# Kernel tuning notes

Measured on AMD Instinct MI355X. Metric: run time of the kernel, lower is better.

Reference implementation:

```python
import jax, jax.numpy as jnp
import numpy as np

B, N, D, H, L = 64, 512, 10, 256, 128  # batch, max_size(nodes), node_dim, hidden, latent
AA, SS, ATOM = 20, 7, 5
K = 2  # conv kernel size
L_KLD = 1e-3


def _lin(k, i, o, s=0.02):
    k1, k2 = jax.random.split(k)
    return jax.random.normal(k1, (i, o), jnp.float32) * s, jax.random.normal(k2, (o,), jnp.float32) * s


def setup_inputs() -> dict:
    key = jax.random.key(0)
    ks = iter(jax.random.split(key, 40))
    nk = lambda: next(ks)
    x = jax.random.normal(nk(), (B, N, D), jnp.float32)
    aa = jax.random.randint(nk(), (B, N), 0, AA + 1).astype(jnp.float32)  # 0 = pad -> ignore_idx
    ss = jax.random.randint(nk(), (B, N), 0, SS + 1).astype(jnp.float32)
    x = x.at[:, :, 0].set(aa).at[:, :, 1].set(ss)
    adj = (jax.random.uniform(nk(), (B, N, N)) < 0.1).astype(jnp.float32)  # sparse binary adjacency
    node_mask = jax.random.randint(nk(), (B, N), 0, 2).astype(bool)
    eps = jax.random.uniform(nk(), (B, N, L), jnp.float32)  # torch.rand_like -> uniform
    W_rel, b_rel = _lin(nk(), D, H)
    W_root, _ = _lin(nk(), D, H)  # lin_root has no bias in DenseSAGEConv
    W_mu, b_mu = _lin(nk(), H, L)
    W_lv, b_lv = _lin(nk(), H, L)
    Wx1, bx1 = _lin(nk(), L, 512); Wx2, bx2 = _lin(nk(), 512, 512); Wx3, bx3 = _lin(nk(), 512, H)
    Wa1, ba1 = _lin(nk(), L, 512); Wa2, ba2 = _lin(nk(), 512, 512); Wa3, ba3 = _lin(nk(), 512, H)
    Wc1 = jax.random.normal(nk(), (256, N, K), jnp.float32) * 0.02; bc1 = jnp.zeros((256,), jnp.float32)
    Wc2 = jax.random.normal(nk(), (N, 256, K), jnp.float32) * 0.02; bc2 = jnp.zeros((N,), jnp.float32)
    W_fcx, b_fcx = _lin(nk(), H, AA * SS)
    W_fca, b_fca = _lin(nk(), H, ATOM)
    W_fcj, b_fcj = _lin(nk(), L - 2 * (K - 1), N)  # cnn out len: 128->127->126
    return dict(x=x, adj=adj, node_mask=node_mask, eps=eps, W_rel=W_rel, b_rel=b_rel, W_root=W_root,
                W_mu=W_mu, b_mu=b_mu, W_lv=W_lv, b_lv=b_lv,
                Wx1=Wx1, bx1=bx1, Wx2=Wx2, bx2=bx2, Wx3=Wx3, bx3=bx3,
                Wa1=Wa1, ba1=ba1, Wa2=Wa2, ba2=ba2, Wa3=Wa3, ba3=ba3,
                Wc1=Wc1, bc1=bc1, Wc2=Wc2, bc2=bc2,
                W_fcx=W_fcx, b_fcx=b_fcx, W_fca=W_fca, b_fca=b_fca, W_fcj=W_fcj, b_fcj=b_fcj)


def reference(x, adj, node_mask, eps, W_rel, b_rel, W_root, W_mu, b_mu, W_lv, b_lv,
              Wx1, bx1, Wx2, bx2, Wx3, bx3, Wa1, ba1, Wa2, ba2, Wa3, ba3,
              Wc1, bc1, Wc2, bc2, W_fcx, b_fcx, W_fca, b_fca, W_fcj, b_fcj):
    relu = jax.nn.relu
    # --- encode: DenseSAGEConv(x, adj, mask) ---
    deg = jnp.clip(jnp.sum(adj, axis=-1, keepdims=True), 1.0, None)
    agg = jnp.einsum('bij,bjd->bid', adj, x) / deg           # [B,N,D]
    h = agg @ W_rel + b_rel + x @ W_root                      # [B,N,H]
    h = h * node_mask[..., None].astype(h.dtype)
    h = relu(h)
    mu = h @ W_mu + b_mu
    lv = h @ W_lv + b_lv
    z = mu + eps * jnp.exp(0.5 * lv)                          # [B,N,L]
    # --- decode ---
    hx = relu(relu(z @ Wx1 + bx1) @ Wx2 + bx2) @ Wx3 + bx3    # gen_x MLP
    ha = relu(relu(z @ Wa1 + ba1) @ Wa2 + ba2) @ Wa3 + ba3    # gen_x_atomic MLP
    dn = ('NCH', 'OIH', 'NCH')
    c = relu(jax.lax.conv_general_dilated(z, Wc1, (1,), 'VALID', dimension_numbers=dn) + bc1[None, :, None])
    c = relu(jax.lax.conv_general_dilated(c, Wc2, (1,), 'VALID', dimension_numbers=dn) + bc2[None, :, None])
    out_x_class = hx @ W_fcx + b_fcx                          # [B,N,AA*SS]
    out_x_atom = ha @ W_fca + b_fca                           # [B,N,ATOM]
    out_adj = c @ W_fcj + b_fcj                               # [B,N,126]@[126,N] -> [B,N,N]
    # --- VAE loss (vectorized _input_classes / _binary_adjacency) ---
    mapping = ((x[..., 1] - 1.0) * AA + (x[..., 0] - 1.0)).astype(jnp.int32)  # [B,N]
    valid = mapping >= 0
    logp = jax.nn.log_softmax(out_x_class, axis=-1)
    ce = -jnp.take_along_axis(logp, jnp.clip(mapping, 0)[..., None], axis=-1)[..., 0]
    ce = jnp.mean(jnp.where(valid, ce, 0.0))
    pair = node_mask[:, :, None] & node_mask[:, None, :]
    eye = jnp.eye(adj.shape[1], dtype=bool)[None]
    adj_bin = (pair & (eye | (adj > 0))).astype(out_adj.dtype)
    l = out_adj
    bce = jnp.mean(jnp.maximum(l, 0.0) - l * adj_bin + jnp.log1p(jnp.exp(-jnp.abs(l))))
    mse = jnp.mean((out_x_atom - x[:, :, ATOM:]) ** 2)
    kl = -0.5 * jnp.sum(1.0 + lv - mu ** 2 - jnp.exp(lv))
    sg = jax.lax.stop_gradient
    beta = jnp.abs((sg(ce) + sg(bce)) / sg(mse))
    loss = ce + beta * mse + bce + L_KLD * kl
    return (loss, out_x_class, out_x_atom, out_adj)
```

## Files before the change

### kernel.cpp

```cpp
#include <hip/hip_runtime.h>
#include <hip/hip_bf16.h>
#include <cstdint>

using bf16x8 = __attribute__((ext_vector_type(8))) __bf16;
using floatx4 = __attribute__((ext_vector_type(4))) float;
typedef unsigned short ushort;

#define Nn  512
#define Dd  10
#define Hh  256
#define Ll  128
#define CLS 140
#define ROWS 32768
#define CH  16384

#define OUT_CLASS 1ull
#define OUT_ATOM  4587521ull
#define OUT_ADJ   4751361ull

#define T1_OFF 12ull
#define T2_OFF (12ull + 16777216ull)
#define HX_OFF (12ull + 33554432ull)
#define WT_OFF 41943068ull
#define AXS_OFF 45088780ull
#define Z_OFF  50331644ull

static __device__ __forceinline__ ushort bfb(float v) {
    __hip_bfloat16 h = __float2bfloat16(v);
    return *reinterpret_cast<ushort*>(&h);
}
static __device__ __forceinline__ float fbf(ushort u) {
    __hip_bfloat16 h = *reinterpret_cast<__hip_bfloat16*>(&u);
    return __bfloat162float(h);
}
static __device__ __forceinline__ unsigned pk2(float a, float b) {
    return (unsigned)bfb(a) | ((unsigned)bfb(b) << 16);
}

struct PDesc { const float* src; ushort* dst; int srcR, srcC, Cp, Kp, tile0, mode; };
struct PTable { PDesc d[12]; };

__global__ __launch_bounds__(256) void prep_kernel(PTable tab) {
    __shared__ float tile[32][33];
    int bt = blockIdx.x, tid = threadIdx.x;
    int di = 0;
    #pragma unroll
    for (int i = 1; i < 12; ++i) if (bt >= tab.d[i].tile0) di = i;
    PDesc d = tab.d[di];
    int lt = bt - d.tile0;
    if (d.mode == 1) {
        long base = (long)lt * 8192;
        const float* s = d.src;
        ushort* o = d.dst;
        for (int i = tid; i < 2048; i += 256) {
            long idx = base + (long)i * 4;
            float4 v = *(const float4*)&s[idx];
            unsigned u0 = pk2(v.x, v.y), u1 = pk2(v.z, v.w);
            *(uint2*)&o[idx] = (uint2){u0, u1};
        }
        return;
    }
    int tilesK = (d.Kp + 31) >> 5;
    int k0 = (lt % tilesK) << 5, n0 = (lt / tilesK) << 5;
    int tx = tid & 31, ty = tid >> 5;
    for (int ky = ty; ky < 32; ky += 8) {
        int k = k0 + ky, n = n0 + tx;
        float v = (k < d.srcR && n < d.srcC) ? d.src[(size_t)k * d.srcC + n] : 0.f;
        tile[ky][tx] = v;
    }
    __syncthreads();
    for (int ny = ty; ny < 32; ny += 8) {
        int n = n0 + ny, k = k0 + tx;
        if (n < d.Cp && k < d.Kp) d.dst[(size_t)n * d.Kp + k] = bfb(tile[tx][ny]);
    }
}

__global__ __launch_bounds__(256, 8) void agg_kernel(
    const float* __restrict__ adj, const float* __restrict__ x,
    float* __restrict__ axs_g)
{
    __shared__ float4 xs4[1536];
    float* xs = (float*)xs4;
    int tid = threadIdx.x;
    int rowbase = blockIdx.x * 16;
    int b = rowbase >> 9, rowloc = rowbase & 511;
    const float* xb = x + (size_t)b * 5120;
    for (int e = tid; e < 6144; e += 256) {
        int j = e / 12, d = e - j * 12;
        xs[e] = (d < 10) ? xb[j * 10 + d] : 0.f;
    }
    __syncthreads();
    int g = tid >> 4, l16 = tid & 15;
    int row = rowbase + g;
    size_t arow = (size_t)row * Nn;
    float accv[10] = {};
    float deg = 0.f;
    for (int it = 0; it < 32; ++it) {
        int j = l16 + (it << 4);
        float a = adj[arow + j];
        if (a != 0.f) {
            deg += a;
            float4 v0 = xs4[j * 3 + 0];
            float4 v1 = xs4[j * 3 + 1];
            float4 v2 = xs4[j * 3 + 2];
            accv[0] += a * v0.x; accv[1] += a * v0.y;
            accv[2] += a * v0.z; accv[3] += a * v0.w;
            accv[4] += a * v1.x; accv[5] += a * v1.y;
            accv[6] += a * v1.z; accv[7] += a * v1.w;
            accv[8] += a * v2.x; accv[9] += a * v2.y;
        }
    }
    #pragma unroll
    for (int o = 8; o > 0; o >>= 1) {
        deg += __shfl_xor(deg, o);
        #pragma unroll
        for (int d = 0; d < 10; ++d) accv[d] += __shfl_xor(accv[d], o);
    }
    float* orow = axs_g + (size_t)row * 20;
    if (l16 == 0) {
        float dg = fmaxf(deg, 1.f);
        #pragma unroll
        for (int d = 0; d < 10; ++d) orow[d] = accv[d] / dg;
    }
    if (l16 < 10) orow[10 + l16] = xs[(rowloc + g) * 12 + l16];
}

__global__ __launch_bounds__(256) void enc2_kernel(
    const float* __restrict__ axs_g,
    const float* __restrict__ Wrel, const float* __restrict__ brel,
    const float* __restrict__ Wroot, const int* __restrict__ nmask,
    const ushort* __restrict__ Wtmu, const float* __restrict__ bmu,
    const ushort* __restrict__ Wtlv, const float* __restrict__ blv,
    const float* __restrict__ eps, float* __restrict__ Z,
    double* __restrict__ acc_kl)
{
    __shared__ float sml[4096];
    __shared__ ushort hsb[16 * 264];
    __shared__ float axs[16][20];
    __shared__ float skred[4];
    int tid = threadIdx.x;
    int rowbase = blockIdx.x * 16;

    for (int e = tid; e < 320; e += 256) ((float*)axs)[e] = axs_g[(size_t)rowbase * 20 + e];
    __syncthreads();

    {
        int c = tid;
        float hacc[16];
        float bb = brel[c];
        #pragma unroll
        for (int r = 0; r < 16; ++r) hacc[r] = bb;
        #pragma unroll
        for (int d = 0; d < 10; ++d) {
            float wr = Wrel[d * Hh + c], wo = Wroot[d * Hh + c];
            #pragma unroll
            for (int r = 0; r < 16; ++r)
                hacc[r] += axs[r][d] * wr + axs[r][10 + d] * wo;
        }
        #pragma unroll
        for (int r = 0; r < 16; ++r) {
            float v = (nmask[rowbase + r] != 0) ? hacc[r] : 0.f;
            hsb[r * 264 + c] = bfb(fmaxf(v, 0.f));
        }
    }
    __syncthreads();

    {
        int lane = tid & 63, wid = tid >> 6;
        int l15 = lane & 15, quad = lane >> 4;
        int half = wid >> 1;
        const ushort* Wt = half ? Wtlv : Wtmu;
        const float* bv = half ? blv : bmu;
        #pragma unroll
        for (int i = 0; i < 4; ++i) {
            int ct = (wid & 1) * 4 + i;
            floatx4 a = (floatx4){0.f, 0.f, 0.f, 0.f};
            #pragma unroll
            for (int k0 = 0; k0 < 8; ++k0) {
                bf16x8 af = __builtin_bit_cast(bf16x8,
                    *(const uint4*)(hsb + l15 * 264 + k0 * 32 + quad * 8));
                bf16x8 bfr = __builtin_bit_cast(bf16x8,
                    *(const uint4*)(Wt + (size_t)(ct * 16 + l15) * 256 + k0 * 32 + quad * 8));
                a = __builtin_amdgcn_mfma_f32_16x16x32_bf16(af, bfr, a, 0, 0, 0);
            }
            int col = ct * 16 + l15;
            float bvv = bv[col];
            #pragma unroll
            for (int r4 = 0; r4 < 4; ++r4) {
                int r = quad * 4 + r4;
                sml[half * 2048 + r * 128 + col] = a[r4] + bvv;
            }
        }
    }
    __syncthreads();

    {
        float kt = 0.f;
        #pragma unroll
        for (int i = 0; i < 8; ++i) {
            int e = tid + i * 256;
            float mu = sml[e], lv = sml[2048 + e];
            float ee = eps[(size_t)rowbase * Ll + e];
            Z[(size_t)rowbase * Ll + e] = mu + ee * expf(0.5f * lv);
            kt += 1.f + lv - mu * mu - expf(lv);
        }
        #pragma unroll
        for (int o = 32; o > 0; o >>= 1) kt += __shfl_xor(kt, o);
        if ((tid & 63) == 0) skred[tid >> 6] = kt;
    }
    __syncthreads();
    if (tid == 0) atomicAdd(acc_kl, (double)(skred[0] + skred[1] + skred[2] + skred[3]));
}

__global__ __launch_bounds__(256) void mgemm_kernel(const void* __restrict__ A, int a_bf16,
                                                    const ushort* __restrict__ Bt,
                                                    const float* __restrict__ bias,
                                                    void* __restrict__ Cp, int c_fp32,
                                                    int N, int K, int ldc, int relu) {
    __shared__ uint4 AsRaw[640];
    __shared__ uint4 BsRaw[640];
    ushort* As = (ushort*)AsRaw;
    ushort* Bs = (ushort*)BsRaw;
    int tid = threadIdx.x;
    int row0 = blockIdx.y << 7, col0 = blockIdx.x << 7;
    int lane = tid & 63, wid = tid >> 6;
    int wm = (wid >> 1) * 64, wn = (wid & 1) * 64;
    int l15 = lane & 15, quad = lane >> 4;
    floatx4 acc[4][4];
    #pragma unroll
    for (int i = 0; i < 4; ++i)
        #pragma unroll
        for (int j = 0; j < 4; ++j) acc[i][j] = (floatx4){0.f, 0.f, 0.f, 0.f};
    int am = tid & 127, aseg = tid >> 7;
    for (int k0 = 0; k0 < K; k0 += 32) {
        {
            uint4* dst = (uint4*)(As + am * 40 + aseg * 16);
            if (a_bf16) {
                const uint4* ap = (const uint4*)((const ushort*)A + (size_t)(row0 + am) * K + k0 + aseg * 16);
                dst[0] = ap[0]; dst[1] = ap[1];
            } else {
                const float4* ap = (const float4*)((const float*)A + (size_t)(row0 + am) * K + k0 + aseg * 16);
                float4 f0 = ap[0], f1 = ap[1], f2 = ap[2], f3 = ap[3];
                dst[0] = (uint4){pk2(f0.x, f0.y), pk2(f0.z, f0.w), pk2(f1.x, f1.y), pk2(f1.z, f1.w)};
                dst[1] = (uint4){pk2(f2.x, f2.y), pk2(f2.z, f2.w), pk2(f3.x, f3.y), pk2(f3.z, f3.w)};
            }
        }
        {
            const uint4* bp = (const uint4*)(Bt + (size_t)(col0 + am) * K + k0 + aseg * 16);
            uint4* dst = (uint4*)(Bs + am * 40 + aseg * 16);
            dst[0] = bp[0]; dst[1] = bp[1];
        }
        __syncthreads();
        bf16x8 af[4], bfv[4];
        #pragma unroll
        for (int mt = 0; mt < 4; ++mt)
            af[mt] = __builtin_bit_cast(bf16x8, *(const uint4*)(As + (wm + mt * 16 + l15) * 40 + quad * 8));
        #pragma unroll
        for (int nt = 0; nt < 4; ++nt)
            bfv[nt] = __builtin_bit_cast(bf16x8, *(const uint4*)(Bs + (wn + nt * 16 + l15) * 40 + quad * 8));
        #pragma unroll
        for (int mt = 0; mt < 4; ++mt)
            #pragma unroll
            for (int nt = 0; nt < 4; ++nt)
                acc[mt][nt] = __builtin_amdgcn_mfma_f32_16x16x32_bf16(af[mt], bfv[nt], acc[mt][nt], 0, 0, 0);
        __syncthreads();
    }
    #pragma unroll
    for (int nt = 0; nt < 4; ++nt) {
        int n = col0 + wn + nt * 16 + l15;
        float bv = bias[n];
        #pragma unroll
        for (int mt = 0; mt < 4; ++mt)
            #pragma unroll
            for (int r = 0; r < 4; ++r) {
                size_t m = row0 + wm + mt * 16 + quad * 4 + r;
                float v = acc[mt][nt][r] + bv;
                if (relu) v = fmaxf(v, 0.f);
                if (c_fp32) ((float*)Cp)[m * ldc + n] = v;
                else ((ushort*)Cp)[m * ldc + n] = bfb(v);
            }
    }
}

__global__ __launch_bounds__(256) void convmfma_kernel(const void* __restrict__ X, int x_bf16,
                                                       long xBS,
                                                       const ushort* __restrict__ Ab,
                                                       const float* __restrict__ bias,
                                                       ushort* __restrict__ Y,
                                                       int Cout, int K, int Tout) {
    __shared__ uint4 AsRaw[640];
    __shared__ uint4 BsRaw[640];
    ushort* As = (ushort*)AsRaw;
    ushort* Bs = (ushort*)BsRaw;
    int tid = threadIdx.x, bz = blockIdx.z;
    int row0 = blockIdx.y << 7;
    int lane = tid & 63, wid = tid >> 6;
    int wm = (wid >> 1) * 64, wn = (wid & 1) * 64;
    int l15 = lane & 15, quad = lane >> 4;
    floatx4 acc[4][4];
    #pragma unroll
    for (int i = 0; i < 4; ++i)
        #pragma unroll
        for (int j = 0; j < 4; ++j) acc[i][j] = (floatx4){0.f, 0.f, 0.f, 0.f};
    int am = tid & 127, aseg = tid >> 7;
    int tnext = (am + 1 > 127) ? 127 : am + 1;
    for (int k0 = 0; k0 < K; k0 += 32) {
        {
            const uint4* ap = (const uint4*)(Ab + (size_t)(row0 + am) * K + k0 + aseg * 16);
            uint4* dst = (uint4*)(As + am * 40 + aseg * 16);
            dst[0] = ap[0]; dst[1] = ap[1];
        }
        {
            unsigned r[8];
            if (x_bf16) {
                const ushort* Xb = (const ushort*)X + (size_t)bz * xBS;
                #pragma unroll
                for (int q = 0; q < 8; ++q) {
                    int kk = k0 + aseg * 16 + 2 * q, i = kk >> 1;
                    r[q] = (unsigned)Xb[i * 128 + am] | ((unsigned)Xb[i * 128 + tnext] << 16);
                }
            } else {
                const float* Xf = (const float*)X + (size_t)bz * xBS;
                #pragma unroll
                for (int q = 0; q < 8; ++q) {
                    int kk = k0 + aseg * 16 + 2 * q, i = kk >> 1;
                    r[q] = pk2(Xf[i * 128 + am], Xf[i * 128 + tnext]);
                }
            }
            uint4* dst = (uint4*)(Bs + am * 40 + aseg * 16);
            dst[0] = (uint4){r[0], r[1], r[2], r[3]};
            dst[1] = (uint4){r[4], r[5], r[6], r[7]};
        }
        __syncthreads();
        bf16x8 af[4], bfv[4];
        #pragma unroll
        for (int mt = 0; mt < 4; ++mt)
            af[mt] = __builtin_bit_cast(bf16x8, *(const uint4*)(As + (wm + mt * 16 + l15) * 40 + quad * 8));
        #pragma unroll
        for (int nt = 0; nt < 4; ++nt)
            bfv[nt] = __builtin_bit_cast(bf16x8, *(const uint4*)(Bs + (wn + nt * 16 + l15) * 40 + quad * 8));
        #pragma unroll
        for (int mt = 0; mt < 4; ++mt)
            #pragma unroll
            for (int nt = 0; nt < 4; ++nt)
                acc[mt][nt] = __builtin_amdgcn_mfma_f32_16x16x32_bf16(af[mt], bfv[nt], acc[mt][nt], 0, 0, 0);
        __syncthreads();
    }
    #pragma unroll
    for (int mt = 0; mt < 4; ++mt)
        #pragma unroll
        for (int r = 0; r < 4; ++r) {
            int m = row0 + wm + mt * 16 + quad * 4 + r;
            float bv = bias[m];
            #pragma unroll
            for (int nt = 0; nt < 4; ++nt) {
                int col = wn + nt * 16 + l15;
                float v = fmaxf(acc[mt][nt][r] + bv, 0.f);
                if (col >= Tout) v = 0.f;
                Y[((size_t)bz * Cout + m) * 128 + col] = bfb(v);
            }
        }
}

__global__ __launch_bounds__(256) void ce_kernel(const ushort* __restrict__ hx,
                                                 const ushort* __restrict__ Wt,
                                                 const float* __restrict__ bfcx,
                                                 const float* __restrict__ x,
                                                 float* __restrict__ out_class,
                                                 double* __restrict__ acc_ce,
                                                 int row0) {
    __shared__ ushort hxb[16 * 264];
    __shared__ float slog[16][144];
    __shared__ float sce[16];
    int tid = threadIdx.x;
    int lbase = blockIdx.x * 16;
    for (int e = tid; e < 512; e += 256) {
        int r = e >> 5, seg = e & 31;
        *(uint4*)(hxb + r * 264 + seg * 8) = *(const uint4*)(hx + (size_t)(lbase + r) * 256 + seg * 8);
    }
    __syncthreads();
    int lane = tid & 63, wid = tid >> 6, l15 = lane & 15, quad = lane >> 4;
    for (int ct = wid; ct < 9; ct += 4) {
        floatx4 a = (floatx4){0.f, 0.f, 0.f, 0.f};
        #pragma unroll
        for (int k0 = 0; k0 < 8; ++k0) {
            bf16x8 af = __builtin_bit_cast(bf16x8, *(const uint4*)(hxb + l15 * 264 + k0 * 32 + quad * 8));
            bf16x8 bfr = __builtin_bit_cast(bf16x8, *(const uint4*)(Wt + (size_t)(ct * 16 + l15) * 256 + k0 * 32 + quad * 8));
            a = __builtin_amdgcn_mfma_f32_16x16x32_bf16(af, bfr, a, 0, 0, 0);
        }
        int col = ct * 16 + l15;
        float bv = (col < CLS) ? bfcx[col] : 0.f;
        #pragma unroll
        for (int r4 = 0; r4 < 4; ++r4) {
            int r = quad * 4 + r4;
            float v = a[r4] + bv;
            slog[r][col] = v;
            if (col < CLS) out_class[(size_t)(row0 + lbase + r) * CLS + col] = v;
        }
    }
    __syncthreads();
    #pragma unroll
    for (int rr = 0; rr < 4; ++rr) {
        int r = wid * 4 + rr;
        float m = -1e30f;
        for (int j = lane; j < CLS; j += 64) m = fmaxf(m, slog[r][j]);
        #pragma unroll
        for (int o = 32; o > 0; o >>= 1) m = fmaxf(m, __shfl_xor(m, o));
        float s = 0.f;
        for (int j = lane; j < CLS; j += 64) s += expf(slog[r][j] - m);
        #pragma unroll
        for (int o = 32; o > 0; o >>= 1) s += __shfl_xor(s, o);
        if (lane == 0) {
            size_t grow = (size_t)row0 + lbase + r;
            float aa = x[grow * Dd + 0];
            float ss = x[grow * Dd + 1];
            int mapping = (int)((ss - 1.f) * 20.f + (aa - 1.f));
            int idx = mapping > 0 ? mapping : 0;
            float ce = -(slog[r][idx] - m - logf(s));
            sce[r] = (mapping < 0) ? 0.f : ce;
        }
    }
    __syncthreads();
    if (tid == 0) {
        float t = 0.f;
        #pragma unroll
        for (int r = 0; r < 16; ++r) t += sce[r];
        atomicAdd(acc_ce, (double)t);
    }
}

__global__ __launch_bounds__(256) void atom_kernel(const ushort* __restrict__ ha,
                                                   const float* __restrict__ Wfca,
                                                   const float* __restrict__ bfca,
                                                   const float* __restrict__ x,
                                                   float* __restrict__ out_atom,
                                                   double* __restrict__ acc_mse,
                                                   int row0) {
    __shared__ double sred[4];
    int tid = threadIdx.x;
    int wid = tid >> 6, lane = tid & 63;
    int rowblk = blockIdx.x * 64;
    double msum = 0.0;
    for (int rr = 0; rr < 16; ++rr) {
        int lrow = rowblk + wid * 16 + rr;
        size_t grow = (size_t)row0 + lrow;
        float acc[5] = {};
        for (int k = lane; k < 256; k += 64) {
            float hv = fbf(ha[(size_t)lrow * Hh + k]);
            #pragma unroll
            for (int o = 0; o < 5; ++o) acc[o] = fmaf(hv, Wfca[k * 5 + o], acc[o]);
        }
        #pragma unroll
        for (int o = 0; o < 5; ++o)
            #pragma unroll
            for (int s = 32; s > 0; s >>= 1) acc[o] += __shfl_xor(acc[o], s);
        if (lane == 0) {
            float ms = 0.f;
            #pragma unroll
            for (int o = 0; o < 5; ++o) {
                float v = acc[o] + bfca[o];
                out_atom[grow * 5 + o] = v;
                float d = v - x[grow * Dd + 5 + o];
                ms += d * d;
            }
            msum += (double)ms;
        }
    }
    if (lane == 0) sred[wid] = msum;
    __syncthreads();
    if (tid == 0) atomicAdd(acc_mse, sred[0] + sred[1] + sred[2] + sred[3]);
}

__global__ __launch_bounds__(256) void bce_kernel(const float* __restrict__ out_adj,
                                                  const float* __restrict__ adj,
                                                  const int* __restrict__ nmask,
                                                  double* __restrict__ acc_bce) {
    __shared__ float sred[4];
    int tid = threadIdx.x;
    float bsum = 0.f;
    for (size_t e = (size_t)blockIdx.x * 256 + tid; e < 16777216ull; e += (size_t)gridDim.x * 256) {
        float l = out_adj[e];
        size_t grow = e >> 9;
        int col = (int)(e & 511);
        int gb = (int)(grow >> 9), n = (int)(grow & 511);
        int mn = nmask[grow];
        int cm = nmask[(size_t)gb * 512 + col];
        float a = adj[e];
        bool abin = (mn != 0) && (cm != 0) && ((col == n) || (a > 0.f));
        bsum += fmaxf(l, 0.f) - (abin ? l : 0.f) + log1pf(expf(-fabsf(l)));
    }
    #pragma unroll
    for (int o = 32; o > 0; o >>= 1) bsum += __shfl_xor(bsum, o);
    if ((tid & 63) == 0) sred[tid >> 6] = bsum;
    __syncthreads();
    if (tid == 0) atomicAdd(acc_bce, (double)(sred[0] + sred[1] + sred[2] + sred[3]));
}

__global__ __launch_bounds__(256) void convgemm_kernel(const float* __restrict__ X,
                                                       const float* __restrict__ Wc,
                                                       const float* __restrict__ bias,
                                                       float* __restrict__ Y,
                                                       int Cin, int Tin, int Cout) {
    __shared__ float As[16][68];
    __shared__ float Bs[16][68];
    int K = Cin * 2, Tout = Tin - 1;
    int tid = threadIdx.x, bz = blockIdx.z;
    const float* Xb = X + (size_t)bz * Cin * Tin;
    int m0 = blockIdx.y << 6, col0 = blockIdx.x << 6;
    int tx = tid & 15, ty = tid >> 4;
    float acc[4][4] = {};
    int sm = tid & 63, sks = (tid >> 6) << 2;
    int bkk = tid >> 4, btof = (tid & 15) << 2;
    for (int k0 = 0; k0 < K; k0 += 16) {
        float4 av = *(const float4*)&Wc[(size_t)(m0 + sm) * K + k0 + sks];
        As[sks + 0][sm] = av.x; As[sks + 1][sm] = av.y;
        As[sks + 2][sm] = av.z; As[sks + 3][sm] = av.w;
        {
            int kg = k0 + bkk, i = kg >> 1, par = kg & 1;
            const float* xr = Xb + (size_t)i * Tin;
            #pragma unroll
            for (int j = 0; j < 4; ++j) {
                int t = col0 + btof + j + par;
                if (t > Tin - 1) t = Tin - 1;
                Bs[bkk][btof + j] = xr[t];
            }
        }
        __syncthreads();
        #pragma unroll
        for (int kk = 0; kk < 16; ++kk) {
            float4 a4 = *(const float4*)&As[kk][ty << 2];
            float4 b4 = *(const float4*)&Bs[kk][tx << 2];
            float a[4] = {a4.x, a4.y, a4.z, a4.w};
            float bb[4] = {b4.x, b4.y, b4.z, b4.w};
            #pragma unroll
            for (int i = 0; i < 4; ++i)
                #pragma unroll
                for (int j = 0; j < 4; ++j)
                    acc[i][j] = fmaf(a[i], bb[j], acc[i][j]);
        }
        __syncthreads();
    }
    #pragma unroll
    for (int i = 0; i < 4; ++i) {
        int m = m0 + (ty << 2) + i;
        float bv = bias[m];
        #pragma unroll
        for (int j = 0; j < 4; ++j) {
            int col = col0 + (tx << 2) + j;
            if (col < Tout)
                Y[((size_t)bz * Cout + m) * Tout + col] = fmaxf(acc[i][j] + bv, 0.f);
        }
    }
}

__global__ __launch_bounds__(256) void adjbce_kernel(const float* __restrict__ c2,
                                                     const float* __restrict__ Wfcj,
                                                     const float* __restrict__ bfcj,
                                                     const float* __restrict__ adj,
                                                     const int* __restrict__ nmask,
                                                     float* __restrict__ out_adj,
                                                     double* __restrict__ acc_bce,
                                                     int b0) {
    __shared__ float cs[8][126];
    __shared__ int smn[8];
    __shared__ float sred[4];
    int tid = threadIdx.x;
    int lbase = blockIdx.x * 8;
    size_t growbase = (size_t)b0 * Nn + lbase;
    int gb = (int)(growbase >> 9);
    for (int e = tid; e < 8 * 126; e += 256) {
        int r = e / 126, k = e - r * 126;
        cs[r][k] = c2[(size_t)(lbase + r) * 126 + k];
    }
    if (tid < 8) smn[tid] = nmask[growbase + tid];
    __syncthreads();
    int j0 = tid, j1 = tid + 256;
    float l0[8], l1[8];
    float bj0 = bfcj[j0], bj1 = bfcj[j1];
    #pragma unroll
    for (int r = 0; r < 8; ++r) { l0[r] = bj0; l1[r] = bj1; }
    for (int k = 0; k < 126; ++k) {
        float w0 = Wfcj[k * Nn + j0];
        float w1 = Wfcj[k * Nn + j1];
        #pragma unroll
        for (int r = 0; r < 8; ++r) {
            float cv = cs[r][k];
            l0[r] = fmaf(cv, w0, l0[r]);
            l1[r] = fmaf(cv, w1, l1[r]);
        }
    }
    int cm0 = nmask[(size_t)(gb << 9) + j0];
    int cm1 = nmask[(size_t)(gb << 9) + j1];
    float bsum = 0.f;
    #pragma unroll
    for (int r = 0; r < 8; ++r) {
        size_t grow = growbase + r;
        int n = (int)(grow & 511);
        int mn = smn[r];
        float a0 = adj[grow * Nn + j0];
        float a1 = adj[grow * Nn + j1];
        out_adj[grow * Nn + j0] = l0[r];
        out_adj[grow * Nn + j1] = l1[r];
        bool ab0 = (mn != 0) && (cm0 != 0) && ((j0 == n) || (a0 > 0.f));
        bool ab1 = (mn != 0) && (cm1 != 0) && ((j1 == n) || (a1 > 0.f));
        bsum += fmaxf(l0[r], 0.f) - (ab0 ? l0[r] : 0.f) + log1pf(expf(-fabsf(l0[r])));
        bsum += fmaxf(l1[r], 0.f) - (ab1 ? l1[r] : 0.f) + log1pf(expf(-fabsf(l1[r])));
    }
    #pragma unroll
    for (int o = 32; o > 0; o >>= 1) bsum += __shfl_xor(bsum, o);
    if ((tid & 63) == 0) sred[tid >> 6] = bsum;
    __syncthreads();
    if (tid == 0) atomicAdd(acc_bce, (double)(sred[0] + sred[1] + sred[2] + sred[3]));
}

__global__ void loss_kernel(const double* __restrict__ acc, float* __restrict__ out) {
    double ce  = acc[0] / 32768.0;
    double bce = acc[1] / 16777216.0;
    double mse = acc[2] / 163840.0;
    double kl  = -0.5 * acc[3];
    double bm = (mse != 0.0) ? fabs(ce + bce) : 0.0;
    out[0] = (float)(ce + bm + bce + 1e-3 * kl);
}

extern "C" void kernel_launch(void* const* d_in, const int* in_sizes, int n_in,
                              void* d_out, int out_size, void* d_ws, size_t ws_size,
                              hipStream_t stream) {
    const float* x      = (const float*)d_in[0];
    const float* adj    = (const float*)d_in[1];
    const int*   nmask  = (const int*)d_in[2];
    const float* eps    = (const float*)d_in[3];
    const float* W_rel  = (const float*)d_in[4];
    const float* b_rel  = (const float*)d_in[5];
    const float* W_root = (const float*)d_in[6];
    const float* W_mu   = (const float*)d_in[7];
    const float* b_mu   = (const float*)d_in[8];
    const float* W_lv   = (const float*)d_in[9];
    const float* b_lv   = (const float*)d_in[10];
    const float* Wx1    = (const float*)d_in[11];
    const float* bx1    = (const float*)d_in[12];
    const float* Wx2    = (const float*)d_in[13];
    const float* bx2    = (const float*)d_in[14];
    const float* Wx3    = (const float*)d_in[15];
    const float* bx3    = (const float*)d_in[16];
    const float* Wa1    = (const float*)d_in[17];
    const float* ba1    = (const float*)d_in[18];
    const float* Wa2    = (const float*)d_in[19];
    const float* ba2    = (const float*)d_in[20];
    const float* Wa3    = (const float*)d_in[21];
    const float* ba3    = (const float*)d_in[22];
    const float* Wc1    = (const float*)d_in[23];
    const float* bc1    = (const float*)d_in[24];
    const float* Wc2    = (const float*)d_in[25];
    const float* bc2    = (const float*)d_in[26];
    const float* W_fcx  = (const float*)d_in[27];
    const float* b_fcx  = (const float*)d_in[28];
    const float* W_fca  = (const float*)d_in[29];
    const float* b_fca  = (const float*)d_in[30];
    const float* W_fcj  = (const float*)d_in[31];
    const float* b_fcj  = (const float*)d_in[32];

    float* out = (float*)d_out;
    char* region = (char*)(out + OUT_ADJ);
    ushort* t1 = (ushort*)(region + T1_OFF);
    ushort* t2 = (ushort*)(region + T2_OFF);
    ushort* hx = (ushort*)(region + HX_OFF);
    float*  Z  = (float*)(region + Z_OFF);
    float*  axs_g = (float*)(region + AXS_OFF);

    ushort* wt_x1  = (ushort*)(region + WT_OFF);
    ushort* wt_x2  = wt_x1 + 65536;
    ushort* wt_x3  = wt_x2 + 262144;
    ushort* wt_a1  = wt_x3 + 131072;
    ushort* wt_a2  = wt_a1 + 65536;
    ushort* wt_a3  = wt_a2 + 262144;
    ushort* wt_mu  = wt_a3 + 131072;
    ushort* wt_lv  = wt_mu + 32768;
    ushort* wt_fcx = wt_lv + 32768;

    double* acc = (double*)d_ws;
    ushort* wc1b   = (ushort*)((char*)d_ws + 256);
    ushort* wc2b   = wc1b + 262144;
    ushort* wt_fcj = wc2b + 262144;
    char* convbuf = (char*)d_ws + 1179904;
    bool fastConv = ws_size >= (size_t)1179904 + 196608;

    hipMemsetAsync(d_ws, 0, 256, stream);

    PTable tab;
    int t0 = 0;
    auto setT = [&](int i, const float* s, ushort* d, int R, int C, int Cp, int Kp) {
        tab.d[i] = {s, d, R, C, Cp, Kp, t0, 0};
        t0 += ((Cp + 31) / 32) * ((Kp + 31) / 32);
    };
    setT(0, Wx1, wt_x1, 128, 512, 512, 128);
    setT(1, Wx2, wt_x2, 512, 512, 512, 512);
    setT(2, Wx3, wt_x3, 512, 256, 256, 512);
    setT(3, Wa1, wt_a1, 128, 512, 512, 128);
    setT(4, Wa2, wt_a2, 512, 512, 512, 512);
    setT(5, Wa3, wt_a3, 512, 256, 256, 512);
    setT(6, W_mu, wt_mu, 256, 128, 128, 256);
    setT(7, W_lv, wt_lv, 256, 128, 128, 256);
    setT(8, W_fcx, wt_fcx, 256, 140, 144, 256);
    setT(9, W_fcj, wt_fcj, 126, 512, 512, 128);
    tab.d[10] = {Wc1, wc1b, 262144, 0, 0, 0, t0, 1}; t0 += 32;
    tab.d[11] = {Wc2, wc2b, 262144, 0, 0, 0, t0, 1}; t0 += 32;
    if (!fastConv) { tab.d[9].src = W_mu; tab.d[9].dst = wt_mu; tab.d[10] = tab.d[9]; tab.d[11] = tab.d[9];
                     tab.d[9].mode = 0; tab.d[10].tile0 = t0 + 999; tab.d[11].tile0 = t0 + 999; t0 = tab.d[9].tile0; }
    prep_kernel<<<fastConv ? 1128 : 960, 256, 0, stream>>>(tab);

    agg_kernel<<<ROWS / 16, 256, 0, stream>>>(adj, x, axs_g);
    enc2_kernel<<<ROWS / 16, 256, 0, stream>>>(axs_g, W_rel, b_rel, W_root, nmask,
                                               wt_mu, b_mu, wt_lv, b_lv, eps, Z, acc + 3);

    for (int c = 0; c < 2; ++c) {
        int r0 = c * CH;
        mgemm_kernel<<<dim3(4, 128), 256, 0, stream>>>(Z + (size_t)r0 * Ll, 0, wt_x1, bx1, t1, 0, 512, 128, 512, 1);
        mgemm_kernel<<<dim3(4, 128), 256, 0, stream>>>(t1, 1, wt_x2, bx2, t2, 0, 512, 512, 512, 1);
        mgemm_kernel<<<dim3(2, 128), 256, 0, stream>>>(t2, 1, wt_x3, bx3, hx, 0, 256, 512, 256, 0);
        ce_kernel<<<CH / 16, 256, 0, stream>>>(hx, wt_fcx, b_fcx, x, out + OUT_CLASS, acc + 0, r0);
    }
    for (int c = 0; c < 2; ++c) {
        int r0 = c * CH;
        mgemm_kernel<<<dim3(4, 128), 256, 0, stream>>>(Z + (size_t)r0 * Ll, 0, wt_a1, ba1, t1, 0, 512, 128, 512, 1);
        mgemm_kernel<<<dim3(4, 128), 256, 0, stream>>>(t1, 1, wt_a2, ba2, t2, 0, 512, 512, 512, 1);
        mgemm_kernel<<<dim3(2, 128), 256, 0, stream>>>(t2, 1, wt_a3, ba3, hx, 0, 256, 512, 256, 0);
        atom_kernel<<<CH / 64, 256, 0, stream>>>(hx, W_fca, b_fca, x, out + OUT_ATOM, acc + 2, r0);
    }

    if (fastConv) {
        size_t avail = ws_size - 1179904;
        int NB = 64;
        while (NB > 1 && (size_t)NB * 196608 > avail) NB >>= 1;
        ushort* c1 = (ushort*)convbuf;
        ushort* c2 = c1 + (size_t)NB * 32768;
        for (int b0 = 0; b0 < 64; b0 += NB) {
            convmfma_kernel<<<dim3(1, 2, NB), 256, 0, stream>>>(Z + (size_t)b0 * 65536, 0, 65536,
                                                               wc1b, bc1, c1, 256, 1024, 127);
            convmfma_kernel<<<dim3(1, 4, NB), 256, 0, stream>>>(c1, 1, 32768,
                                                               wc2b, bc2, c2, 512, 512, 126);
            mgemm_kernel<<<dim3(4, NB * 4), 256, 0, stream>>>(c2, 1, wt_fcj, b_fcj,
                                                              out + OUT_ADJ + (size_t)b0 * 262144, 1,
                                                              512, 128, 512, 0);
        }
        bce_kernel<<<1024, 256, 0, stream>>>(out + OUT_ADJ, adj, nmask, acc + 1);
    } else {
        size_t avail = (ws_size > 256) ? ws_size - 256 : 0;
        int NB = 64;
        while (NB > 1 && (size_t)NB * 388096 > avail) NB >>= 1;
        float* c1 = (float*)((char*)d_ws + 256);
        float* c2 = (float*)((char*)d_ws + 256 + (size_t)NB * 256 * 127 * 4);
        for (int b0 = 0; b0 < 64; b0 += NB) {
            convgemm_kernel<<<dim3(2, 4, NB), 256, 0, stream>>>(Z + (size_t)b0 * 65536, Wc1, bc1, c1, 512, 128, 256);
            convgemm_kernel<<<dim3(2, 8, NB), 256, 0, stream>>>(c1, Wc2, bc2, c2, 256, 127, 512);
            adjbce_kernel<<<NB * Nn / 8, 256, 0, stream>>>(c2, W_fcj, b_fcj, adj, nmask,
                                                           out + OUT_ADJ, acc + 1, b0);
        }
    }

    loss_kernel<<<1, 1, 0, stream>>>(acc, out);
}
```

Measured before the change: 919.9 us.

## Move SAGE encoder projection to split-bf16 MFMA and fuse mu/logvar epilogue

Replaces the scalar FP32 DenseSAGEConv projection in the encoder kernel with MFMA ops. Inputs and weights are split into bf16 high and low parts (three MFMAs) to keep near-FP32 accuracy, and the packed weights are built in the prep kernel. The mu/logvar GEMM is restructured so each wave computes both outputs and applies reparameterization and the KL term straight from registers, which drops the fp32 shared staging buffer and one barrier. This cuts shared memory and raises the occupancy hint, at the cost of extra prep work and some approximation error from the split-bf16 scheme.

```diff
diff --git a/kernel.cpp b/kernel.cpp
--- a/kernel.cpp
+++ b/kernel.cpp
@@ -38,14 +38,14 @@
 }
 
 struct PDesc { const float* src; ushort* dst; int srcR, srcC, Cp, Kp, tile0, mode; };
-struct PTable { PDesc d[12]; };
+struct PTable { PDesc d[18]; };
 
 __global__ __launch_bounds__(256) void prep_kernel(PTable tab) {
     __shared__ float tile[32][33];
     int bt = blockIdx.x, tid = threadIdx.x;
     int di = 0;
     #pragma unroll
-    for (int i = 1; i < 12; ++i) if (bt >= tab.d[i].tile0) di = i;
+    for (int i = 1; i < 18; ++i) if (bt >= tab.d[i].tile0) di = i;
     PDesc d = tab.d[di];
     int lt = bt - d.tile0;
     if (d.mode == 1) {
@@ -71,7 +71,18 @@
     __syncthreads();
     for (int ny = ty; ny < 32; ny += 8) {
         int n = n0 + ny, k = k0 + tx;
-        if (n < d.Cp && k < d.Kp) d.dst[(size_t)n * d.Kp + k] = bfb(tile[tx][ny]);
+        if (n < d.Cp && k < d.Kp) {
+            float v = tile[tx][ny];
+            if (d.mode >= 64) {
+                int koff = d.mode - 64;
+                ushort u;
+                if (koff >= 32) u = bfb(v - fbf(bfb(v)));
+                else u = bfb(v);
+                d.dst[(size_t)n * 64 + koff + k] = u;
+            } else {
+                d.dst[(size_t)n * d.Kp + k] = bfb(v);
+            }
+        }
     }
 }
 
@@ -125,89 +136,97 @@
     if (l16 < 10) orow[10 + l16] = xs[(rowloc + g) * 12 + l16];
 }
 
-__global__ __launch_bounds__(256) void enc2_kernel(
+__global__ __launch_bounds__(256, 4) void enc2_kernel(
     const float* __restrict__ axs_g,
-    const float* __restrict__ Wrel, const float* __restrict__ brel,
-    const float* __restrict__ Wroot, const int* __restrict__ nmask,
+    const ushort* __restrict__ Wenc,
+    const float* __restrict__ brel, const int* __restrict__ nmask,
     const ushort* __restrict__ Wtmu, const float* __restrict__ bmu,
     const ushort* __restrict__ Wtlv, const float* __restrict__ blv,
     const float* __restrict__ eps, float* __restrict__ Z,
     double* __restrict__ acc_kl)
 {
-    __shared__ float sml[4096];
-    __shared__ ushort hsb[16 * 264];
-    __shared__ float axs[16][20];
+    __shared__ uint4 axsbRaw[160];
+    __shared__ uint4 hsbRaw[528];
+    __shared__ int smask[16];
     __shared__ float skred[4];
+    ushort* axsb = (ushort*)axsbRaw;
+    ushort* hsb = (ushort*)hsbRaw;
     int tid = threadIdx.x;
     int rowbase = blockIdx.x * 16;
-
-    for (int e = tid; e < 320; e += 256) ((float*)axs)[e] = axs_g[(size_t)rowbase * 20 + e];
-    __syncthreads();
+    size_t abase = (size_t)rowbase * 20;
+
+    for (int e = tid; e < 1280; e += 256) {
+        int r = e / 80, d = e - r * 80;
+        ushort u = 0;
+        if (d < 20) {
+            u = bfb(axs_g[abase + r * 20 + d]);
+        } else if (d >= 40 && d < 60) {
+            float v = axs_g[abase + r * 20 + d - 40];
+            u = bfb(v - fbf(bfb(v)));
+        }
+        axsb[e] = u;
+    }
+    if (tid < 16) smask[tid] = nmask[rowbase + tid];
+    __syncthreads();
+
+    int lane = tid & 63, wid = tid >> 6;
+    int l15 = lane & 15, quad = lane >> 4;
 
     {
-        int c = tid;
-        float hacc[16];
-        float bb = brel[c];
-        #pragma unroll
-        for (int r = 0; r < 16; ++r) hacc[r] = bb;
-        #pragma unroll
-        for (int d = 0; d < 10; ++d) {
-            float wr = Wrel[d * Hh + c], wo = Wroot[d * Hh + c];
-            #pragma unroll
-            for (int r = 0; r < 16; ++r)
-                hacc[r] += axs[r][d] * wr + axs[r][10 + d] * wo;
-        }
-        #pragma unroll
-        for (int r = 0; r < 16; ++r) {
-            float v = (nmask[rowbase + r] != 0) ? hacc[r] : 0.f;
-            hsb[r * 264 + c] = bfb(fmaxf(v, 0.f));
-        }
-    }
-    __syncthreads();
-
-    {
-        int lane = tid & 63, wid = tid >> 6;
-        int l15 = lane & 15, quad = lane >> 4;
-        int half = wid >> 1;
-        const ushort* Wt = half ? Wtlv : Wtmu;
-        const float* bv = half ? blv : bmu;
+        bf16x8 ah = __builtin_bit_cast(bf16x8, *(const uint4*)(axsb + l15 * 80 + quad * 8));
+        bf16x8 al = __builtin_bit_cast(bf16x8, *(const uint4*)(axsb + l15 * 80 + 40 + quad * 8));
         #pragma unroll
         for (int i = 0; i < 4; ++i) {
-            int ct = (wid & 1) * 4 + i;
+            int ct = wid * 4 + i;
+            int col = ct * 16 + l15;
+            bf16x8 bh = __builtin_bit_cast(bf16x8, *(const uint4*)(Wenc + (size_t)col * 64 + quad * 8));
+            bf16x8 blo = __builtin_bit_cast(bf16x8, *(const uint4*)(Wenc + (size_t)col * 64 + 32 + quad * 8));
             floatx4 a = (floatx4){0.f, 0.f, 0.f, 0.f};
-            #pragma unroll
-            for (int k0 = 0; k0 < 8; ++k0) {
-                bf16x8 af = __builtin_bit_cast(bf16x8,
-                    *(const uint4*)(hsb + l15 * 264 + k0 * 32 + quad * 8));
-                bf16x8 bfr = __builtin_bit_cast(bf16x8,
-                    *(const uint4*)(Wt + (size_t)(ct * 16 + l15) * 256 + k0 * 32 + quad * 8));
-                a = __builtin_amdgcn_mfma_f32_16x16x32_bf16(af, bfr, a, 0, 0, 0);
+            a = __builtin_amdgcn_mfma_f32_16x16x32_bf16(al, bh, a, 0, 0, 0);
+            a = __builtin_amdgcn_mfma_f32_16x16x32_bf16(ah, blo, a, 0, 0, 0);
+            a = __builtin_amdgcn_mfma_f32_16x16x32_bf16(ah, bh, a, 0, 0, 0);
+            float bb = brel[col];
+            #pragma unroll
+            for (int r4 = 0; r4 < 4; ++r4) {
+                int row = quad * 4 + r4;
+                float v = a[r4] + bb;
+                v = (smask[row] != 0) ? fmaxf(v, 0.f) : 0.f;
+                hsb[row * 264 + col] = bfb(v);
             }
-            int col = ct * 16 + l15;
-            float bvv = bv[col];
-            #pragma unroll
-            for (int r4 = 0; r4 < 4; ++r4) {
-                int r = quad * 4 + r4;
-                sml[half * 2048 + r * 128 + col] = a[r4] + bvv;
-            }
-        }
-    }
-    __syncthreads();
-
-    {
-        float kt = 0.f;
-        #pragma unroll
-        for (int i = 0; i < 8; ++i) {
-            int e = tid + i * 256;
-            float mu = sml[e], lv = sml[2048 + e];
-            float ee = eps[(size_t)rowbase * Ll + e];
-            Z[(size_t)rowbase * Ll + e] = mu + ee * expf(0.5f * lv);
+        }
+    }
+    __syncthreads();
+
+    float kt = 0.f;
+    #pragma unroll
+    for (int i = 0; i < 2; ++i) {
+        int ct = wid * 2 + i;
+        int col = ct * 16 + l15;
+        floatx4 amu = (floatx4){0.f, 0.f, 0.f, 0.f};
+        floatx4 alv = (floatx4){0.f, 0.f, 0.f, 0.f};
+        #pragma unroll
+        for (int k0 = 0; k0 < 8; ++k0) {
+            bf16x8 af = __builtin_bit_cast(bf16x8, *(const uint4*)(hsb + l15 * 264 + k0 * 32 + quad * 8));
+            bf16x8 bm = __builtin_bit_cast(bf16x8, *(const uint4*)(Wtmu + (size_t)col * 256 + k0 * 32 + quad * 8));
+            bf16x8 bl = __builtin_bit_cast(bf16x8, *(const uint4*)(Wtlv + (size_t)col * 256 + k0 * 32 + quad * 8));
+            amu = __builtin_amdgcn_mfma_f32_16x16x32_bf16(af, bm, amu, 0, 0, 0);
+            alv = __builtin_amdgcn_mfma_f32_16x16x32_bf16(af, bl, alv, 0, 0, 0);
+        }
+        float bmv = bmu[col], blv_ = blv[col];
+        #pragma unroll
+        for (int r4 = 0; r4 < 4; ++r4) {
+            int row = quad * 4 + r4;
+            size_t zi = ((size_t)rowbase + row) * Ll + col;
+            float mu = amu[r4] + bmv;
+            float lv = alv[r4] + blv_;
+            float ee = eps[zi];
+            Z[zi] = mu + ee * expf(0.5f * lv);
             kt += 1.f + lv - mu * mu - expf(lv);
         }
-        #pragma unroll
-        for (int o = 32; o > 0; o >>= 1) kt += __shfl_xor(kt, o);
-        if ((tid & 63) == 0) skred[tid >> 6] = kt;
-    }
+    }
+    #pragma unroll
+    for (int o = 32; o > 0; o >>= 1) kt += __shfl_xor(kt, o);
+    if (lane == 0) skred[wid] = kt;
     __syncthreads();
     if (tid == 0) atomicAdd(acc_kl, (double)(skred[0] + skred[1] + skred[2] + skred[3]));
 }
@@ -676,6 +695,7 @@
     ushort* wt_mu  = wt_a3 + 131072;
     ushort* wt_lv  = wt_mu + 32768;
     ushort* wt_fcx = wt_lv + 32768;
+    ushort* wt_enc = wt_fcx + 36864;
 
     double* acc = (double*)d_ws;
     ushort* wc1b   = (ushort*)((char*)d_ws + 256);
@@ -700,16 +720,21 @@
     setT(5, Wa3, wt_a3, 512, 256, 256, 512);
     setT(6, W_mu, wt_mu, 256, 128, 128, 256);
     setT(7, W_lv, wt_lv, 256, 128, 128, 256);
-    setT(8, W_fcx, wt_fcx, 256, 140, 144, 256);
-    setT(9, W_fcj, wt_fcj, 126, 512, 512, 128);
-    tab.d[10] = {Wc1, wc1b, 262144, 0, 0, 0, t0, 1}; t0 += 32;
-    tab.d[11] = {Wc2, wc2b, 262144, 0, 0, 0, t0, 1}; t0 += 32;
-    if (!fastConv) { tab.d[9].src = W_mu; tab.d[9].dst = wt_mu; tab.d[10] = tab.d[9]; tab.d[11] = tab.d[9];
-                     tab.d[9].mode = 0; tab.d[10].tile0 = t0 + 999; tab.d[11].tile0 = t0 + 999; t0 = tab.d[9].tile0; }
-    prep_kernel<<<fastConv ? 1128 : 960, 256, 0, stream>>>(tab);
+    setT(8,  W_rel,  wt_enc, 10, 256, 256, 10); tab.d[8].mode  = 64 + 0;
+    setT(9,  W_root, wt_enc, 10, 256, 256, 10); tab.d[9].mode  = 64 + 10;
+    setT(10, W_rel,  wt_enc, 0,  0,   256, 12); tab.d[10].mode = 64 + 20;
+    setT(11, W_rel,  wt_enc, 10, 256, 256, 10); tab.d[11].mode = 64 + 32;
+    setT(12, W_root, wt_enc, 10, 256, 256, 10); tab.d[12].mode = 64 + 42;
+    setT(13, W_rel,  wt_enc, 0,  0,   256, 12); tab.d[13].mode = 64 + 52;
+    setT(14, W_fcx, wt_fcx, 256, 140, 144, 256);
+    int t_nofcj = t0;
+    setT(15, W_fcj, wt_fcj, 126, 512, 512, 128);
+    tab.d[16] = {Wc1, wc1b, 262144, 0, 0, 0, t0, 1}; t0 += 32;
+    tab.d[17] = {Wc2, wc2b, 262144, 0, 0, 0, t0, 1}; t0 += 32;
+    prep_kernel<<<fastConv ? t0 : t_nofcj, 256, 0, stream>>>(tab);
 
     agg_kernel<<<ROWS / 16, 256, 0, stream>>>(adj, x, axs_g);
-    enc2_kernel<<<ROWS / 16, 256, 0, stream>>>(axs_g, W_rel, b_rel, W_root, nmask,
+    enc2_kernel<<<ROWS / 16, 256, 0, stream>>>(axs_g, wt_enc, b_rel, nmask,
                                                wt_mu, b_mu, wt_lv, b_lv, eps, Z, acc + 3);
 
     for (int c = 0; c < 2; ++c) {
```

After: 877.3 us. 4.6% less time.
